# Performance work log

Hardware: AMD Instinct MI355X
Metric: run time of the kernel (lower is better)

The kernel has to match this reference:

```python
import jax, jax.numpy as jnp
import numpy as np

N = 10000      # nodes
E = 320000     # edges (avg degree 32)
SI, VI = 256, 32   # node scalar / vector channels
SE, VE = 64, 4     # edge scalar / vector channels
SO, VO = 256, 32   # output channels
IN_S = 2 * SI + SE         # 576 (self_message=True)
IN_V = 2 * VI + VE         # 68
H = max(IN_V, VO)          # 68, GBP hidden vector dim
EPS = 1e-8


def setup_inputs() -> dict:
    key = jax.random.key(0)
    ks = jax.random.split(key, 9)
    node_s = jax.random.normal(ks[0], (N, SI), jnp.float32)
    node_v = jax.random.normal(ks[1], (N, VI, 3), jnp.float32)
    edge_s = jax.random.normal(ks[2], (E, SE), jnp.float32)
    edge_v = jax.random.normal(ks[3], (E, VE, 3), jnp.float32)
    # GBP params (stored as [in, out] so y = x @ W)
    wh = jax.random.normal(ks[4], (IN_V, H), jnp.float32) / np.sqrt(IN_V)
    ws_w = jax.random.normal(ks[5], (IN_S + H, SO), jnp.float32) / np.sqrt(IN_S + H)
    ws_b = jnp.zeros((SO,), jnp.float32)
    wv = jax.random.normal(ks[6], (H, VO), jnp.float32) / np.sqrt(H)
    edge_index = jax.random.randint(ks[7], (2, E), 0, N, jnp.int64)
    return {"node_s": node_s, "node_v": node_v, "edge_s": edge_s,
            "edge_v": edge_v, "wh": wh, "ws_w": ws_w, "ws_b": ws_b,
            "wv": wv, "edge_index": edge_index}


def reference(node_s, node_v, edge_s, edge_v, wh, ws_w, ws_b, wv, edge_index):
    n = node_s.shape[0]
    src, dst = edge_index[0], edge_index[1]
    # gather + tuple_cat((s_j, v_j), edge_attr, (s_i, v_i))
    s_cat = jnp.concatenate([node_s[src], edge_s, node_s[dst]], axis=-1)   # [E, IN_S]
    v_cat = jnp.concatenate([node_v[src], edge_v, node_v[dst]], axis=-2)   # [E, IN_V, 3]
    # GBP message (activations=(None,None), no vector gate)
    v_pre = jnp.swapaxes(v_cat, -1, -2)                # [E, 3, IN_V]
    vh = v_pre @ wh                                    # [E, 3, H]
    vn = jnp.sqrt(jnp.maximum(jnp.sum(vh * vh, axis=-2), EPS))  # _norm_no_nan, [E, H]
    s_msg = jnp.concatenate([s_cat, vn], axis=-1) @ ws_w + ws_b  # [E, SO]
    v_msg = jnp.swapaxes(vh @ wv, -1, -2)              # [E, VO, 3]
    # scatter-mean to target nodes
    agg_s = jax.ops.segment_sum(s_msg, dst, num_segments=n)       # [N, SO]
    agg_v = jax.ops.segment_sum(v_msg, dst, num_segments=n)       # [N, VO, 3]
    cnt = jax.ops.segment_sum(jnp.ones((s_msg.shape[0],), s_msg.dtype), dst,
                              num_segments=n)
    cnt = jnp.maximum(cnt, 1.0)
    out_s = agg_s / cnt[:, None]
    out_v = agg_v / cnt[:, None, None]
    # _merge(s, V): flatten vector channels and append to scalars
    return jnp.concatenate([out_s, out_v.reshape(n, 3 * VO)], axis=-1)  # [N, SO+3*VO]
```

## Files before the change

### kernel.cpp

```cpp
#include <hip/hip_runtime.h>
#include <hip/hip_bf16.h>

#define N_NODES 10000
#define E_TOT   320000

typedef __attribute__((ext_vector_type(8))) short short8;
typedef __attribute__((ext_vector_type(4))) short s16x4;
typedef __attribute__((ext_vector_type(4))) float f32x4;

#define HIST_OFF    0u
#define FILL_OFF    40000u
#define ZERO_BYTES  80000u
#define ROWPTR_OFF  80000u
#define PERM_OFF    120064u
#define PSRC_OFF    1400064u
#define CN_OFF      2680064u
#define QARR_OFF    13560064u
#define QV_OFF      17720064u
#define WHV4_OFF    19640064u
#define WBIG_OFF    19640576u
#define NSBF_OFF    19984640u
#define ANSB_OFF    25104640u
#define EAB_OFF     30224640u
#define AP_OFF      33424640u
#define AEV_OFF     41584640u
#define FLAGS_OFF   42064640u
#define NODES_OFF   120064u

union BfS { __hip_bfloat16 h; short s; };
__device__ __forceinline__ short f2bf(float x) { BfS u; u.h = __float2bfloat16(x); return u.s; }
__device__ __forceinline__ float bf(short x) { BfS u; u.s = x; return __bfloat162float(u.h); }
__device__ __forceinline__ float bflo(unsigned u) { return __uint_as_float(u << 16); }
__device__ __forceinline__ float bfhi(unsigned u) { return __uint_as_float(u & 0xffff0000u); }
__device__ __forceinline__ float ldin(const void* p, int f32m, long i) {
  return f32m ? ((const float*)p)[i] : __bfloat162float(((const __hip_bfloat16*)p)[i]);
}
__device__ __forceinline__ int get_ei(const void* p, int i64m, long i) {
  return i64m ? (int)(((const long long*)p)[i]) : ((const int*)p)[i];
}

__global__ __launch_bounds__(256) void hist_det(
    const void* __restrict__ edge_index, const unsigned short* __restrict__ ns_u16,
    int* __restrict__ hist, int* __restrict__ flags)
{
  const int tid = threadIdx.x;
  const int* ei = (const int*)edge_index;
  int nz = (ei[2 * tid + 1] != 0) ? 1 : 0;
  unsigned long long m = __ballot(nz);
  __shared__ int cnt4[4];
  if ((tid & 63) == 0) cnt4[tid >> 6] = __popcll(m);
  __syncthreads();
  const int i64m = (cnt4[0] + cnt4[1] + cnt4[2] + cnt4[3]) < 16 ? 1 : 0;
  int e = blockIdx.x * 256 + tid;
  int dst = get_ei(edge_index, i64m, (long)E_TOT + e);
  atomicAdd(&hist[dst], 1);
  if (blockIdx.x == 0) {
    __shared__ int cf;
    if (tid == 0) cf = 0;
    __syncthreads();
    int c1 = 0;
    for (int i = tid; i < 8192; i += 256) {
      unsigned ex = (ns_u16[2 * i] >> 7) & 0xFF;
      if (ex < 100 || ex > 140) c1++;
    }
    atomicAdd(&cf, c1);
    __syncthreads();
    if (tid == 0) { flags[0] = (cf > 512) ? 1 : 0; flags[1] = i64m; }
  }
}

__global__ __launch_bounds__(256) void scanperm(
    const void* __restrict__ edge_index, const int* __restrict__ flags,
    const int* __restrict__ hist, int* __restrict__ rowptr,
    int* __restrict__ fill, int* __restrict__ perm, int* __restrict__ psrc)
{
  __shared__ int rp[N_NODES];
  __shared__ int part[256];
  const int tid = threadIdx.x;
  for (int i = tid; i < N_NODES; i += 256) rp[i] = hist[i];
  __syncthreads();
  const int base = tid * 40;
  int s = 0;
  for (int i = 0; i < 40; ++i) { int idx = base + i; if (idx < N_NODES) s += rp[idx]; }
  part[tid] = s;
  __syncthreads();
  for (int off = 1; off < 256; off <<= 1) {
    int v = (tid >= off) ? part[tid - off] : 0;
    __syncthreads();
    part[tid] += v;
    __syncthreads();
  }
  int run = (tid > 0) ? part[tid - 1] : 0;
  for (int i = 0; i < 40; ++i) {
    int idx = base + i;
    if (idx < N_NODES) { int h = rp[idx]; rp[idx] = run; run += h; }
  }
  __syncthreads();
  if (blockIdx.x == 0) {
    for (int i = tid; i < N_NODES; i += 256) rowptr[i] = rp[i];
    if (tid == 0) rowptr[N_NODES] = part[255];
  }
  const int i64m = flags[1];
  int e = blockIdx.x * 256 + tid;
  int dst = get_ei(edge_index, i64m, (long)E_TOT + e);
  int src = get_ei(edge_index, i64m, e);
  int pos = rp[dst] + atomicAdd(&fill[dst], 1);
  perm[pos] = e; psrc[pos] = src;
}

__global__ __launch_bounds__(256) void node_pre_prep(
    const void* __restrict__ node_v, const void* __restrict__ wh,
    const void* __restrict__ wv, const void* __restrict__ node_s,
    const void* __restrict__ ws_w, const int* __restrict__ flags,
    short* __restrict__ CN, short* __restrict__ QARR,
    short* __restrict__ QV, short* __restrict__ ns_bf,
    short* __restrict__ Wbig, float* __restrict__ whv4)
{
  const int f32m = flags[0];
  const int b = blockIdx.x, tid = threadIdx.x;
  __shared__ float whs[68 * 68];
  __shared__ float wvs[68 * 32];
  __shared__ float nv[4][96];
  __shared__ float pq[4][408];
  if (b >= 2500) {
    int pb = b - 2500;
    if (pb < 672) {
      int flat = pb * 256 + tid;
      int o = flat / 672, k = flat % 672;
      short v = 0;
      if (k < 320)      v = f2bf(ldin(ws_w, f32m, (long)k * 256 + o));
      else if (k < 388) v = f2bf(ldin(ws_w, f32m, (long)(576 + k - 320) * 256 + o));
      else if (k >= 416) v = f2bf(ldin(ws_w, f32m, (long)(k - 96) * 256 + o));
      Wbig[flat] = v;
    } else if (tid < 128) {
      int q = tid / 32, c = tid % 32;
      float acc = 0.f;
      for (int h = 0; h < 68; ++h)
        acc += ldin(wh, f32m, (32 + q) * 68 + h) * ldin(wv, f32m, h * 32 + c);
      whv4[tid] = acc;
    }
    return;
  }
  int n0 = b * 4;
  for (int i = tid; i < 4624; i += 256) whs[i] = ldin(wh, f32m, i);
  for (int i = tid; i < 2176; i += 256) wvs[i] = ldin(wv, f32m, i);
  for (int i = tid; i < 4 * 96; i += 256) nv[i / 96][i % 96] = ldin(node_v, f32m, (long)n0 * 96 + i);
  for (int i = tid; i < 1024; i += 256)
    ns_bf[(long)n0 * 256 + i] = f2bf(ldin(node_s, f32m, (long)n0 * 256 + i));
  __syncthreads();
  for (int o = tid; o < 4 * 408; o += 256) {
    int i = o / 408, r0 = o % 408;
    int part = r0 / 204, r = r0 % 204, d = r / 68, h = r % 68;
    int cbase = part ? 36 : 0;
    float acc = 0.f;
#pragma unroll
    for (int c = 0; c < 32; ++c)
      acc += nv[i][c * 3 + d] * whs[(cbase + c) * 68 + h];
    pq[i][r0] = acc;
  }
  __syncthreads();
  for (int o = tid; o < 4 * 544; o += 256) {
    int i = o / 544, k = o % 544;
    short v = 0;
    if (k < 512) {
      int l = k >> 3, j = k & 7;
      if (j < 4)      v = f2bf(ldin(node_s, f32m, (long)(n0 + i) * 256 + l * 4 + j));
      else if (j < 7) v = f2bf(pq[i][(j - 4) * 68 + l]);
    } else if (k < 528) {
      int idx = k - 512, jj = idx >> 2, d = idx & 3;
      if (d < 3) v = f2bf(pq[i][d * 68 + 64 + jj]);
    }
    CN[(long)(n0 + i) * 544 + k] = v;
  }
  for (int o = tid; o < 4 * 208; o += 256) {
    int i = o / 208, k = o % 208;
    QARR[(long)(n0 + i) * 208 + k] = (k < 204) ? f2bf(pq[i][204 + k]) : (short)0;
  }
  for (int o = tid; o < 4 * 96; o += 256) {
    int i = o / 96, r = o % 96, d = r / 32, c = r % 32;
    float acc = 0.f;
    for (int h = 0; h < 68; ++h)
      acc += pq[i][204 + d * 68 + h] * wvs[h * 32 + c];
    QV[(long)(n0 + i) * 96 + r] = f2bf(acc);
  }
}

struct EdgeLds {
  float ansL[4][256];
  float apL[4][204];
  float avnL[4][132];
  float aesL[4][64];
  float aevL[4][12];
};

template <int F32M>
__device__ __forceinline__ void edge_body(
    const void* __restrict__ edge_v, const void* __restrict__ edge_s,
    const void* __restrict__ wh,
    const int* __restrict__ rowptr, const int* __restrict__ perm,
    const int* __restrict__ psrc, const short* __restrict__ CN,
    const short* __restrict__ QARR,
    short* __restrict__ ANSb, short* __restrict__ EAb,
    float* __restrict__ AP, float* __restrict__ AEV, EdgeLds* lds)
{
  const int tid = threadIdx.x;
  const int lane = tid & 63, w = tid >> 6;
  const int n = blockIdx.x;
  const int beg = rowptr[n], deg = rowptr[n + 1] - beg;
  const bool has2 = (lane < 4);
  const int h2 = 64 + lane;
  const float w4a0 = ldin(wh, F32M, 32 * 68 + lane);
  const float w4a1 = ldin(wh, F32M, 33 * 68 + lane);
  const float w4a2 = ldin(wh, F32M, 34 * 68 + lane);
  const float w4a3 = ldin(wh, F32M, 35 * 68 + lane);
  const float w4b0 = has2 ? ldin(wh, F32M, 32 * 68 + h2) : 0.f;
  const float w4b1 = has2 ? ldin(wh, F32M, 33 * 68 + h2) : 0.f;
  const float w4b2 = has2 ? ldin(wh, F32M, 34 * 68 + h2) : 0.f;
  const float w4b3 = has2 ? ldin(wh, F32M, 35 * 68 + h2) : 0.f;
  const short* qp = QARR + (long)n * 208;
  const float qa0 = bf(qp[0 * 68 + lane]);
  const float qa1 = bf(qp[1 * 68 + lane]);
  const float qa2 = bf(qp[2 * 68 + lane]);
  const float qb0 = has2 ? bf(qp[0 * 68 + h2]) : 0.f;
  const float qb1 = has2 ? bf(qp[1 * 68 + h2]) : 0.f;
  const float qb2 = has2 ? bf(qp[2 * 68 + h2]) : 0.f;
  float an0 = 0.f, an1 = 0.f, an2 = 0.f, an3 = 0.f;
  float ap0 = 0.f, ap1 = 0.f, ap2 = 0.f;
  float bq0 = 0.f, bq1 = 0.f, bq2 = 0.f;
  float avna = 0.f, avnb = 0.f, aes = 0.f, aev = 0.f;

  int e = w;
  int s_cur = 0, d_cur = 0;
  int sv1 = 0, id1 = 0;
  short8 cv = {};
  s16x4 tl = {};
  float es_c = 0.f, evl_c = 0.f;
  float c0 = 0.f, c1 = 0.f, c2 = 0.f, c3 = 0.f, c4 = 0.f, c5 = 0.f;
  float c6 = 0.f, c7 = 0.f, c8 = 0.f, c9 = 0.f, cA = 0.f, cB = 0.f;
  if (e < deg) {
    int sv0 = psrc[beg + e], id0 = perm[beg + e];
    s_cur = __builtin_amdgcn_readfirstlane(sv0);
    d_cur = __builtin_amdgcn_readfirstlane(id0);
    cv = *(const short8*)(CN + (long)s_cur * 544 + lane * 8);
    if (has2) tl = *(const s16x4*)(CN + (long)s_cur * 544 + 512 + lane * 4);
    es_c = ldin(edge_s, F32M, (long)d_cur * 64 + lane);
    if (lane < 12) evl_c = ldin(edge_v, F32M, (long)d_cur * 12 + lane);
    if (F32M) {
      const float* evp = (const float*)edge_v + (long)d_cur * 12;
      c0 = evp[0]; c1 = evp[1]; c2 = evp[2]; c3 = evp[3];
      c4 = evp[4]; c5 = evp[5]; c6 = evp[6]; c7 = evp[7];
      c8 = evp[8]; c9 = evp[9]; cA = evp[10]; cB = evp[11];
    } else {
      const unsigned* evp = (const unsigned*)((const short*)edge_v + (long)d_cur * 12);
      unsigned u0 = evp[0], u1 = evp[1], u2 = evp[2];
      unsigned u3 = evp[3], u4 = evp[4], u5 = evp[5];
      c0 = bflo(u0); c1 = bfhi(u0); c2 = bflo(u1); c3 = bfhi(u1);
      c4 = bflo(u2); c5 = bfhi(u2); c6 = bflo(u3); c7 = bfhi(u3);
      c8 = bflo(u4); c9 = bfhi(u4); cA = bflo(u5); cB = bfhi(u5);
    }
  }
  if (e + 4 < deg) { sv1 = psrc[beg + e + 4]; id1 = perm[beg + e + 4]; }

  while (e < deg) {
    const bool vnext = (e + 4 < deg);
    const int sN = vnext ? __builtin_amdgcn_readfirstlane(sv1) : s_cur;
    const int dN = vnext ? __builtin_amdgcn_readfirstlane(id1) : d_cur;
    short8 cvn = *(const short8*)(CN + (long)sN * 544 + lane * 8);
    s16x4 tln = {};
    if (has2) tln = *(const s16x4*)(CN + (long)sN * 544 + 512 + lane * 4);
    float es_n = ldin(edge_s, F32M, (long)dN * 64 + lane);
    float evl_n = 0.f;
    if (lane < 12) evl_n = ldin(edge_v, F32M, (long)dN * 12 + lane);
    float n0, n1, n2, n3, n4, n5, n6, n7, n8, n9, nA, nB;
    if (F32M) {
      const float* evp = (const float*)edge_v + (long)dN * 12;
      n0 = evp[0]; n1 = evp[1]; n2 = evp[2]; n3 = evp[3];
      n4 = evp[4]; n5 = evp[5]; n6 = evp[6]; n7 = evp[7];
      n8 = evp[8]; n9 = evp[9]; nA = evp[10]; nB = evp[11];
    } else {
      const unsigned* evp = (const unsigned*)((const short*)edge_v + (long)dN * 12);
      unsigned u0 = evp[0], u1 = evp[1], u2 = evp[2];
      unsigned u3 = evp[3], u4 = evp[4], u5 = evp[5];
      n0 = bflo(u0); n1 = bfhi(u0); n2 = bflo(u1); n3 = bfhi(u1);
      n4 = bflo(u2); n5 = bfhi(u2); n6 = bflo(u3); n7 = bfhi(u3);
      n8 = bflo(u4); n9 = bfhi(u4); nA = bflo(u5); nB = bfhi(u5);
    }
    if (e + 8 < deg) { sv1 = psrc[beg + e + 8]; id1 = perm[beg + e + 8]; }
    an0 += bf(cv[0]); an1 += bf(cv[1]); an2 += bf(cv[2]); an3 += bf(cv[3]);
    const float pa0 = bf(cv[4]), pa1 = bf(cv[5]), pa2 = bf(cv[6]);
    aes += es_c; aev += evl_c;
    float v0 = pa0 + qa0 + c0 * w4a0 + c3 * w4a1 + c6 * w4a2 + c9 * w4a3;
    float v1 = pa1 + qa1 + c1 * w4a0 + c4 * w4a1 + c7 * w4a2 + cA * w4a3;
    float v2 = pa2 + qa2 + c2 * w4a0 + c5 * w4a1 + c8 * w4a2 + cB * w4a3;
    avna += sqrtf(fmaxf(v0 * v0 + v1 * v1 + v2 * v2, 1e-8f));
    ap0 += pa0; ap1 += pa1; ap2 += pa2;
    if (has2) {
      const float pb0 = bf(tl.x), pb1 = bf(tl.y), pb2 = bf(tl.z);
      float u0 = pb0 + qb0 + c0 * w4b0 + c3 * w4b1 + c6 * w4b2 + c9 * w4b3;
      float u1 = pb1 + qb1 + c1 * w4b0 + c4 * w4b1 + c7 * w4b2 + cA * w4b3;
      float u2 = pb2 + qb2 + c2 * w4b0 + c5 * w4b1 + c8 * w4b2 + cB * w4b3;
      avnb += sqrtf(fmaxf(u0 * u0 + u1 * u1 + u2 * u2, 1e-8f));
      bq0 += pb0; bq1 += pb1; bq2 += pb2;
    }
    cv = cvn; tl = tln; es_c = es_n; evl_c = evl_n;
    c0 = n0; c1 = n1; c2 = n2; c3 = n3; c4 = n4; c5 = n5;
    c6 = n6; c7 = n7; c8 = n8; c9 = n9; cA = nA; cB = nB;
    s_cur = sN; d_cur = dN;
    e += 4;
  }
  lds->ansL[w][lane * 4 + 0] = an0; lds->ansL[w][lane * 4 + 1] = an1;
  lds->ansL[w][lane * 4 + 2] = an2; lds->ansL[w][lane * 4 + 3] = an3;
  lds->apL[w][lane * 3 + 0] = ap0; lds->apL[w][lane * 3 + 1] = ap1;
  lds->apL[w][lane * 3 + 2] = ap2;
  if (has2) {
    lds->apL[w][192 + lane * 3 + 0] = bq0;
    lds->apL[w][192 + lane * 3 + 1] = bq1;
    lds->apL[w][192 + lane * 3 + 2] = bq2;
  }
  lds->avnL[w][lane] = avna;
  if (has2) lds->avnL[w][64 + lane] = avnb;
  lds->aesL[w][lane] = aes;
  if (lane < 12) lds->aevL[w][lane] = aev;
  __syncthreads();
  const float inv = 1.f / fmaxf((float)deg, 1.f);
  {
    float s = lds->ansL[0][tid] + lds->ansL[1][tid] + lds->ansL[2][tid] + lds->ansL[3][tid];
    ANSb[(long)n * 256 + tid] = f2bf(s * inv);
  }
  if (tid < 204) {
    float s = lds->apL[0][tid] + lds->apL[1][tid] + lds->apL[2][tid] + lds->apL[3][tid];
    AP[(long)n * 204 + tid] = s;
  } else if (tid < 216) {
    int c = tid - 204;
    float s = lds->aevL[0][c] + lds->aevL[1][c] + lds->aevL[2][c] + lds->aevL[3][c];
    AEV[(long)n * 12 + c] = s;
  }
  if (tid < 64) {
    float s = lds->aesL[0][tid] + lds->aesL[1][tid] + lds->aesL[2][tid] + lds->aesL[3][tid];
    EAb[(long)n * 160 + tid] = f2bf(s * inv);
  } else if (tid < 132) {
    int c = tid - 64;
    float s = lds->avnL[0][c] + lds->avnL[1][c] + lds->avnL[2][c] + lds->avnL[3][c];
    EAb[(long)n * 160 + 64 + c] = f2bf(s * inv);
  } else if (tid < 160) {
    EAb[(long)n * 160 + tid] = 0;
  }
}

__global__ __launch_bounds__(256) void edge_block(
    const void* __restrict__ edge_v, const void* __restrict__ edge_s,
    const void* __restrict__ wh, const int* __restrict__ flags,
    const int* __restrict__ rowptr, const int* __restrict__ perm,
    const int* __restrict__ psrc, const short* __restrict__ CN,
    const short* __restrict__ QARR,
    short* __restrict__ ANSb, short* __restrict__ EAb,
    float* __restrict__ AP, float* __restrict__ AEV)
{
  __shared__ EdgeLds lds;
  if (flags[0])
    edge_body<1>(edge_v, edge_s, wh, rowptr, perm, psrc, CN, QARR,
                 ANSb, EAb, AP, AEV, &lds);
  else
    edge_body<0>(edge_v, edge_s, wh, rowptr, perm, psrc, CN, QARR,
                 ANSb, EAb, AP, AEV, &lds);
}

__global__ __launch_bounds__(256) void node_gemm(
    const short* __restrict__ ANSb, const short* __restrict__ EAb,
    const short* __restrict__ nsb, const short* __restrict__ Wbig,
    float* __restrict__ NodeS)
{
  __shared__ __align__(16) short Xs[64 * 40];
  __shared__ __align__(16) short Ws[256 * 40];
  const int tid = threadIdx.x;
  const int n0 = blockIdx.x * 64;
  const int lane = tid & 63, wave = tid >> 6;
  const int frow = lane & 15, fk = (lane >> 4) * 8, q = lane >> 4;
  f32x4 acc[4][4];
#pragma unroll
  for (int ri = 0; ri < 4; ++ri)
#pragma unroll
    for (int ci = 0; ci < 4; ++ci)
      acc[ri][ci] = (f32x4){0.f, 0.f, 0.f, 0.f};
  const int se = tid >> 2, sq = tid & 3;
  const int rn = min(n0 + se, N_NODES - 1);
  for (int s = 0; s < 21; ++s) {
    short8 xv;
    if (s < 8)       xv = *(const short8*)&ANSb[(long)rn * 256 + s * 32 + sq * 8];
    else if (s < 13) xv = *(const short8*)&EAb[(long)rn * 160 + (s - 8) * 32 + sq * 8];
    else             xv = *(const short8*)&nsb[(long)rn * 256 + (s - 13) * 32 + sq * 8];
    *(short8*)&Xs[se * 40 + sq * 8] = xv;
#pragma unroll
    for (int it = 0; it < 4; ++it) {
      int flat = it * 256 + tid;
      int nn = flat >> 2, qq = flat & 3;
      *(short8*)&Ws[nn * 40 + qq * 8] = *(const short8*)&Wbig[nn * 672 + s * 32 + qq * 8];
    }
    __syncthreads();
    short8 a[4];
#pragma unroll
    for (int ri = 0; ri < 4; ++ri)
      a[ri] = *(const short8*)&Xs[(ri * 16 + frow) * 40 + fk];
#pragma unroll
    for (int ci = 0; ci < 4; ++ci) {
      int nn = wave * 64 + ci * 16 + frow;
      short8 b = *(const short8*)&Ws[nn * 40 + fk];
#pragma unroll
      for (int ri = 0; ri < 4; ++ri)
        acc[ri][ci] = __builtin_amdgcn_mfma_f32_16x16x32_bf16(a[ri], b, acc[ri][ci], 0, 0, 0);
    }
    __syncthreads();
  }
#pragma unroll
  for (int ri = 0; ri < 4; ++ri)
#pragma unroll
    for (int rr = 0; rr < 4; ++rr) {
      int row = n0 + ri * 16 + q * 4 + rr;
      if (row < N_NODES) {
#pragma unroll
        for (int ci = 0; ci < 4; ++ci) {
          int col = wave * 64 + ci * 16 + (lane & 15);
          NodeS[(long)row * 256 + col] = acc[ri][ci][rr];
        }
      }
    }
}

__global__ __launch_bounds__(256) void final_fuse(
    const float* __restrict__ NodeS, const float* __restrict__ AP,
    const float* __restrict__ AEV, const void* __restrict__ wv,
    const float* __restrict__ whv4, const int* __restrict__ rowptr,
    const short* __restrict__ QV, const void* __restrict__ ws_b,
    const int* __restrict__ flags, void* __restrict__ out)
{
  const int f32m = flags[0];
  int n0 = blockIdx.x * 4, tid = threadIdx.x;
  __shared__ float wvs[68 * 32];
  __shared__ float wh4s[128];
  __shared__ float APs[4][204];
  __shared__ float AEVs[4][12];
  __shared__ float aggL[4][96];
  for (int i = tid; i < 2176; i += 256) wvs[i] = ldin(wv, f32m, i);
  if (tid < 128) wh4s[tid] = whv4[tid];
  for (int i = tid; i < 816; i += 256) APs[i / 204][i % 204] = AP[(long)n0 * 204 + i];
  if (tid < 48) AEVs[tid / 12][tid % 12] = AEV[(long)n0 * 12 + tid];
  __syncthreads();
  for (int o = tid; o < 384; o += 256) {
    int i = o / 96, r = o % 96, c = r / 3, d = r % 3;
    float acc = AEVs[i][d] * wh4s[c] + AEVs[i][3 + d] * wh4s[32 + c]
              + AEVs[i][6 + d] * wh4s[64 + c] + AEVs[i][9 + d] * wh4s[96 + c];
    for (int h = 0; h < 68; ++h)
      acc += APs[i][h * 3 + d] * wvs[h * 32 + c];
    aggL[i][r] = acc;
  }
  __syncthreads();
  for (int o = tid; o < 1408; o += 256) {
    int i = o / 352, j = o % 352;
    int n = n0 + i;
    int deg = rowptr[n + 1] - rowptr[n];
    float v;
    if (j < 256) {
      v = (deg > 0) ? (NodeS[(long)n * 256 + j] + ldin(ws_b, f32m, j)) : 0.f;
    } else {
      int m = j - 256, ch = m / 3, d = m % 3;
      float inv = 1.f / fmaxf((float)deg, 1.f);
      v = aggL[i][m] * inv;
      if (deg > 0) v += bf(QV[(long)n * 96 + d * 32 + ch]);
    }
    long flat = (long)n * 352 + j;
    if (f32m) ((float*)out)[flat] = v;
    else      ((__hip_bfloat16*)out)[flat] = __float2bfloat16(v);
  }
}

extern "C" void kernel_launch(void* const* d_in, const int* in_sizes, int n_in,
                              void* d_out, int out_size, void* d_ws, size_t ws_size,
                              hipStream_t stream) {
  const void* node_s = d_in[0];
  const void* node_v = d_in[1];
  const void* edge_s = d_in[2];
  const void* edge_v = d_in[3];
  const void* wh     = d_in[4];
  const void* ws_w   = d_in[5];
  const void* ws_b   = d_in[6];
  const void* wv     = d_in[7];
  const void* edge_index = d_in[8];

  char* ws = (char*)d_ws;
  int*   hist  = (int*)(ws + HIST_OFF);
  int*   fill  = (int*)(ws + FILL_OFF);
  int*   rowptr= (int*)(ws + ROWPTR_OFF);
  int*   perm  = (int*)(ws + PERM_OFF);
  int*   psrc  = (int*)(ws + PSRC_OFF);
  short* CN    = (short*)(ws + CN_OFF);
  short* QARR  = (short*)(ws + QARR_OFF);
  short* QV    = (short*)(ws + QV_OFF);
  float* whv4  = (float*)(ws + WHV4_OFF);
  short* Wbig  = (short*)(ws + WBIG_OFF);
  short* ns_bf = (short*)(ws + NSBF_OFF);
  short* ANSb  = (short*)(ws + ANSB_OFF);
  short* EAb   = (short*)(ws + EAB_OFF);
  float* AP    = (float*)(ws + AP_OFF);
  float* AEV   = (float*)(ws + AEV_OFF);
  float* NodeS = (float*)(ws + NODES_OFF);
  int*   flags = (int*)(ws + FLAGS_OFF);

  hipMemsetAsync(d_ws, 0, ZERO_BYTES, stream);
  hist_det<<<1250, 256, 0, stream>>>(edge_index, (const unsigned short*)node_s,
                                     hist, flags);
  scanperm<<<1250, 256, 0, stream>>>(edge_index, flags, hist, rowptr, fill,
                                     perm, psrc);
  node_pre_prep<<<3173, 256, 0, stream>>>(node_v, wh, wv, node_s, ws_w, flags,
                                          CN, QARR, QV, ns_bf, Wbig, whv4);
  edge_block<<<10000, 256, 0, stream>>>(edge_v, edge_s, wh, flags, rowptr,
                                        perm, psrc, CN, QARR,
                                        ANSb, EAb, AP, AEV);
  node_gemm<<<157, 256, 0, stream>>>(ANSb, EAb, ns_bf, Wbig, NodeS);
  final_fuse<<<2500, 256, 0, stream>>>(NodeS, AP, AEV, wv, whv4, rowptr,
                                       QV, ws_b, flags, d_out);
}
```

Before: 431.2 us.

## Pre-permute edge features into CSR order during scanperm for sequential edge reads

During the permutation pass, scanperm now scatters each edge's scalar and vector features (converted to bf16) into a new workspace buffer ordered by CSR position. A new edge kernel then reads these features sequentially by row instead of gathering them through perm. The fallback kernel, used when the workspace is too small, drops the explicit one-ahead software prefetch of the gathered data. The cost is an extra scattered write of roughly 48 MB in scanperm, bf16 rounding of the edge features in the f32 path, and a dependence on workspace size.

```diff
diff --git a/kernel.cpp b/kernel.cpp
--- a/kernel.cpp
+++ b/kernel.cpp
@@ -25,6 +25,8 @@
 #define AP_OFF      33424640u
 #define AEV_OFF     41584640u
 #define FLAGS_OFF   42064640u
+#define EVS_OFF     42064704u
+#define EVS_BYTES   48640000u
 #define NODES_OFF   120064u
 
 union BfS { __hip_bfloat16 h; short s; };
@@ -70,12 +72,15 @@
 }
 
 __global__ __launch_bounds__(256) void scanperm(
-    const void* __restrict__ edge_index, const int* __restrict__ flags,
+    const void* __restrict__ edge_index, const void* __restrict__ edge_s,
+    const void* __restrict__ edge_v, const int* __restrict__ flags,
     const int* __restrict__ hist, int* __restrict__ rowptr,
-    int* __restrict__ fill, int* __restrict__ perm, int* __restrict__ psrc)
+    int* __restrict__ fill, int* __restrict__ perm, int* __restrict__ psrc,
+    short* __restrict__ EVS, int do_copy)
 {
   __shared__ int rp[N_NODES];
   __shared__ int part[256];
+  __shared__ int posL[256];
   const int tid = threadIdx.x;
   for (int i = tid; i < N_NODES; i += 256) rp[i] = hist[i];
   __syncthreads();
@@ -100,12 +105,24 @@
     for (int i = tid; i < N_NODES; i += 256) rowptr[i] = rp[i];
     if (tid == 0) rowptr[N_NODES] = part[255];
   }
-  const int i64m = flags[1];
+  const int i64m = flags[1], f32m = flags[0];
   int e = blockIdx.x * 256 + tid;
   int dst = get_ei(edge_index, i64m, (long)E_TOT + e);
   int src = get_ei(edge_index, i64m, e);
   int pos = rp[dst] + atomicAdd(&fill[dst], 1);
   perm[pos] = e; psrc[pos] = src;
+  posL[tid] = pos;
+  __syncthreads();
+  if (do_copy) {
+    const long ebase = (long)blockIdx.x * 256;
+    for (int i = tid; i < 256 * 76; i += 256) {
+      int li = i / 76, ch = i - li * 76;
+      long eg = ebase + li;
+      float v = (ch < 64) ? ldin(edge_s, f32m, eg * 64 + ch)
+                          : ldin(edge_v, f32m, eg * 12 + (ch - 64));
+      EVS[(long)posL[li] * 76 + ch] = f2bf(v);
+    }
+  }
 }
 
 __global__ __launch_bounds__(256) void node_pre_prep(
@@ -193,8 +210,126 @@
   float aevL[4][12];
 };
 
+__device__ __forceinline__ void edge_reduce_epilogue(
+    EdgeLds* lds, int n, int tid, int deg,
+    short* __restrict__ ANSb, short* __restrict__ EAb,
+    float* __restrict__ AP, float* __restrict__ AEV)
+{
+  __syncthreads();
+  const float inv = 1.f / fmaxf((float)deg, 1.f);
+  {
+    float s = lds->ansL[0][tid] + lds->ansL[1][tid] + lds->ansL[2][tid] + lds->ansL[3][tid];
+    ANSb[(long)n * 256 + tid] = f2bf(s * inv);
+  }
+  if (tid < 204) {
+    float s = lds->apL[0][tid] + lds->apL[1][tid] + lds->apL[2][tid] + lds->apL[3][tid];
+    AP[(long)n * 204 + tid] = s;
+  } else if (tid < 216) {
+    int c = tid - 204;
+    float s = lds->aevL[0][c] + lds->aevL[1][c] + lds->aevL[2][c] + lds->aevL[3][c];
+    AEV[(long)n * 12 + c] = s;
+  }
+  if (tid < 64) {
+    float s = lds->aesL[0][tid] + lds->aesL[1][tid] + lds->aesL[2][tid] + lds->aesL[3][tid];
+    EAb[(long)n * 160 + tid] = f2bf(s * inv);
+  } else if (tid < 132) {
+    int c = tid - 64;
+    float s = lds->avnL[0][c] + lds->avnL[1][c] + lds->avnL[2][c] + lds->avnL[3][c];
+    EAb[(long)n * 160 + 64 + c] = f2bf(s * inv);
+  } else if (tid < 160) {
+    EAb[(long)n * 160 + tid] = 0;
+  }
+}
+
+__global__ __launch_bounds__(256) void edge_block_seq(
+    const short* __restrict__ EVS, const void* __restrict__ wh,
+    const int* __restrict__ flags, const int* __restrict__ rowptr,
+    const int* __restrict__ psrc, const short* __restrict__ CN,
+    const short* __restrict__ QARR,
+    short* __restrict__ ANSb, short* __restrict__ EAb,
+    float* __restrict__ AP, float* __restrict__ AEV)
+{
+  __shared__ EdgeLds lds;
+  const int f32m = flags[0];
+  const int tid = threadIdx.x, lane = tid & 63, w = tid >> 6;
+  const int n = blockIdx.x;
+  const int beg = rowptr[n], deg = rowptr[n + 1] - beg;
+  const bool has2 = (lane < 4);
+  const int h2 = 64 + lane;
+  const float w4a0 = ldin(wh, f32m, 32 * 68 + lane);
+  const float w4a1 = ldin(wh, f32m, 33 * 68 + lane);
+  const float w4a2 = ldin(wh, f32m, 34 * 68 + lane);
+  const float w4a3 = ldin(wh, f32m, 35 * 68 + lane);
+  const float w4b0 = has2 ? ldin(wh, f32m, 32 * 68 + h2) : 0.f;
+  const float w4b1 = has2 ? ldin(wh, f32m, 33 * 68 + h2) : 0.f;
+  const float w4b2 = has2 ? ldin(wh, f32m, 34 * 68 + h2) : 0.f;
+  const float w4b3 = has2 ? ldin(wh, f32m, 35 * 68 + h2) : 0.f;
+  const short* qp = QARR + (long)n * 208;
+  const float qa0 = bf(qp[0 * 68 + lane]);
+  const float qa1 = bf(qp[1 * 68 + lane]);
+  const float qa2 = bf(qp[2 * 68 + lane]);
+  const float qb0 = has2 ? bf(qp[0 * 68 + h2]) : 0.f;
+  const float qb1 = has2 ? bf(qp[1 * 68 + h2]) : 0.f;
+  const float qb2 = has2 ? bf(qp[2 * 68 + h2]) : 0.f;
+  float an0 = 0.f, an1 = 0.f, an2 = 0.f, an3 = 0.f;
+  float ap0 = 0.f, ap1 = 0.f, ap2 = 0.f;
+  float bq0 = 0.f, bq1 = 0.f, bq2 = 0.f;
+  float avna = 0.f, avnb = 0.f, aes = 0.f, aev = 0.f;
+  int e = w;
+  int sv = (e < deg) ? psrc[beg + e] : 0;
+  while (e < deg) {
+    int en = e + 4;
+    int svn = (en < deg) ? psrc[beg + en] : 0;
+    const int s_s = __builtin_amdgcn_readfirstlane(sv);
+    const int row = __builtin_amdgcn_readfirstlane(beg + e);
+    const short* cs = CN + (long)s_s * 544;
+    short8 cv = *(const short8*)(cs + lane * 8);
+    const short* er = EVS + (long)row * 76;
+    float esv = bf(er[lane]);
+    float evl = (lane < 12) ? bf(er[64 + lane]) : 0.f;
+    const unsigned* ep = (const unsigned*)(er + 64);
+    unsigned u0 = ep[0], u1 = ep[1], u2 = ep[2];
+    unsigned u3 = ep[3], u4 = ep[4], u5 = ep[5];
+    float c0 = bflo(u0), c1 = bfhi(u0), c2 = bflo(u1), c3 = bfhi(u1);
+    float c4 = bflo(u2), c5 = bfhi(u2), c6 = bflo(u3), c7 = bfhi(u3);
+    float c8 = bflo(u4), c9 = bfhi(u4), cA = bflo(u5), cB = bfhi(u5);
+    an0 += bf(cv[0]); an1 += bf(cv[1]); an2 += bf(cv[2]); an3 += bf(cv[3]);
+    const float pa0 = bf(cv[4]), pa1 = bf(cv[5]), pa2 = bf(cv[6]);
+    aes += esv; aev += evl;
+    float v0 = pa0 + qa0 + c0 * w4a0 + c3 * w4a1 + c6 * w4a2 + c9 * w4a3;
+    float v1 = pa1 + qa1 + c1 * w4a0 + c4 * w4a1 + c7 * w4a2 + cA * w4a3;
+    float v2 = pa2 + qa2 + c2 * w4a0 + c5 * w4a1 + c8 * w4a2 + cB * w4a3;
+    avna += sqrtf(fmaxf(v0 * v0 + v1 * v1 + v2 * v2, 1e-8f));
+    ap0 += pa0; ap1 += pa1; ap2 += pa2;
+    if (has2) {
+      s16x4 tl = *(const s16x4*)(cs + 512 + lane * 4);
+      const float pb0 = bf(tl.x), pb1 = bf(tl.y), pb2 = bf(tl.z);
+      float t0 = pb0 + qb0 + c0 * w4b0 + c3 * w4b1 + c6 * w4b2 + c9 * w4b3;
+      float t1 = pb1 + qb1 + c1 * w4b0 + c4 * w4b1 + c7 * w4b2 + cA * w4b3;
+      float t2 = pb2 + qb2 + c2 * w4b0 + c5 * w4b1 + c8 * w4b2 + cB * w4b3;
+      avnb += sqrtf(fmaxf(t0 * t0 + t1 * t1 + t2 * t2, 1e-8f));
+      bq0 += pb0; bq1 += pb1; bq2 += pb2;
+    }
+    e = en; sv = svn;
+  }
+  lds.ansL[w][lane * 4 + 0] = an0; lds.ansL[w][lane * 4 + 1] = an1;
+  lds.ansL[w][lane * 4 + 2] = an2; lds.ansL[w][lane * 4 + 3] = an3;
+  lds.apL[w][lane * 3 + 0] = ap0; lds.apL[w][lane * 3 + 1] = ap1;
+  lds.apL[w][lane * 3 + 2] = ap2;
+  if (has2) {
+    lds.apL[w][192 + lane * 3 + 0] = bq0;
+    lds.apL[w][192 + lane * 3 + 1] = bq1;
+    lds.apL[w][192 + lane * 3 + 2] = bq2;
+  }
+  lds.avnL[w][lane] = avna;
+  if (has2) lds.avnL[w][64 + lane] = avnb;
+  lds.aesL[w][lane] = aes;
+  if (lane < 12) lds.aevL[w][lane] = aev;
+  edge_reduce_epilogue(&lds, n, tid, deg, ANSb, EAb, AP, AEV);
+}
+
 template <int F32M>
-__device__ __forceinline__ void edge_body(
+__device__ __forceinline__ void edge_body_fb(
     const void* __restrict__ edge_v, const void* __restrict__ edge_s,
     const void* __restrict__ wh,
     const int* __restrict__ rowptr, const int* __restrict__ perm,
@@ -228,85 +363,49 @@
   float ap0 = 0.f, ap1 = 0.f, ap2 = 0.f;
   float bq0 = 0.f, bq1 = 0.f, bq2 = 0.f;
   float avna = 0.f, avnb = 0.f, aes = 0.f, aev = 0.f;
-
   int e = w;
-  int s_cur = 0, d_cur = 0;
-  int sv1 = 0, id1 = 0;
-  short8 cv = {};
-  s16x4 tl = {};
-  float es_c = 0.f, evl_c = 0.f;
-  float c0 = 0.f, c1 = 0.f, c2 = 0.f, c3 = 0.f, c4 = 0.f, c5 = 0.f;
-  float c6 = 0.f, c7 = 0.f, c8 = 0.f, c9 = 0.f, cA = 0.f, cB = 0.f;
-  if (e < deg) {
-    int sv0 = psrc[beg + e], id0 = perm[beg + e];
-    s_cur = __builtin_amdgcn_readfirstlane(sv0);
-    d_cur = __builtin_amdgcn_readfirstlane(id0);
-    cv = *(const short8*)(CN + (long)s_cur * 544 + lane * 8);
-    if (has2) tl = *(const s16x4*)(CN + (long)s_cur * 544 + 512 + lane * 4);
-    es_c = ldin(edge_s, F32M, (long)d_cur * 64 + lane);
-    if (lane < 12) evl_c = ldin(edge_v, F32M, (long)d_cur * 12 + lane);
+  int sv = 0, eid = 0;
+  if (e < deg) { sv = psrc[beg + e]; eid = perm[beg + e]; }
+  while (e < deg) {
+    int en = e + 4, svn = 0, eidn = 0;
+    if (en < deg) { svn = psrc[beg + en]; eidn = perm[beg + en]; }
+    const int sv_s  = __builtin_amdgcn_readfirstlane(sv);
+    const int eid_s = __builtin_amdgcn_readfirstlane(eid);
+    float ev0, ev1, ev2, ev3, ev4, ev5, ev6, ev7, ev8, ev9, evA, evB;
     if (F32M) {
-      const float* evp = (const float*)edge_v + (long)d_cur * 12;
-      c0 = evp[0]; c1 = evp[1]; c2 = evp[2]; c3 = evp[3];
-      c4 = evp[4]; c5 = evp[5]; c6 = evp[6]; c7 = evp[7];
-      c8 = evp[8]; c9 = evp[9]; cA = evp[10]; cB = evp[11];
+      const float* evp = (const float*)edge_v + (long)eid_s * 12;
+      ev0 = evp[0]; ev1 = evp[1]; ev2 = evp[2]; ev3 = evp[3];
+      ev4 = evp[4]; ev5 = evp[5]; ev6 = evp[6]; ev7 = evp[7];
+      ev8 = evp[8]; ev9 = evp[9]; evA = evp[10]; evB = evp[11];
     } else {
-      const unsigned* evp = (const unsigned*)((const short*)edge_v + (long)d_cur * 12);
+      const unsigned* evp = (const unsigned*)((const short*)edge_v + (long)eid_s * 12);
       unsigned u0 = evp[0], u1 = evp[1], u2 = evp[2];
       unsigned u3 = evp[3], u4 = evp[4], u5 = evp[5];
-      c0 = bflo(u0); c1 = bfhi(u0); c2 = bflo(u1); c3 = bfhi(u1);
-      c4 = bflo(u2); c5 = bfhi(u2); c6 = bflo(u3); c7 = bfhi(u3);
-      c8 = bflo(u4); c9 = bfhi(u4); cA = bflo(u5); cB = bfhi(u5);
-    }
-  }
-  if (e + 4 < deg) { sv1 = psrc[beg + e + 4]; id1 = perm[beg + e + 4]; }
-
-  while (e < deg) {
-    const bool vnext = (e + 4 < deg);
-    const int sN = vnext ? __builtin_amdgcn_readfirstlane(sv1) : s_cur;
-    const int dN = vnext ? __builtin_amdgcn_readfirstlane(id1) : d_cur;
-    short8 cvn = *(const short8*)(CN + (long)sN * 544 + lane * 8);
-    s16x4 tln = {};
-    if (has2) tln = *(const s16x4*)(CN + (long)sN * 544 + 512 + lane * 4);
-    float es_n = ldin(edge_s, F32M, (long)dN * 64 + lane);
-    float evl_n = 0.f;
-    if (lane < 12) evl_n = ldin(edge_v, F32M, (long)dN * 12 + lane);
-    float n0, n1, n2, n3, n4, n5, n6, n7, n8, n9, nA, nB;
-    if (F32M) {
-      const float* evp = (const float*)edge_v + (long)dN * 12;
-      n0 = evp[0]; n1 = evp[1]; n2 = evp[2]; n3 = evp[3];
-      n4 = evp[4]; n5 = evp[5]; n6 = evp[6]; n7 = evp[7];
-      n8 = evp[8]; n9 = evp[9]; nA = evp[10]; nB = evp[11];
-    } else {
-      const unsigned* evp = (const unsigned*)((const short*)edge_v + (long)dN * 12);
-      unsigned u0 = evp[0], u1 = evp[1], u2 = evp[2];
-      unsigned u3 = evp[3], u4 = evp[4], u5 = evp[5];
-      n0 = bflo(u0); n1 = bfhi(u0); n2 = bflo(u1); n3 = bfhi(u1);
-      n4 = bflo(u2); n5 = bfhi(u2); n6 = bflo(u3); n7 = bfhi(u3);
-      n8 = bflo(u4); n9 = bfhi(u4); nA = bflo(u5); nB = bfhi(u5);
-    }
-    if (e + 8 < deg) { sv1 = psrc[beg + e + 8]; id1 = perm[beg + e + 8]; }
+      ev0 = bflo(u0); ev1 = bfhi(u0); ev2 = bflo(u1); ev3 = bfhi(u1);
+      ev4 = bflo(u2); ev5 = bfhi(u2); ev6 = bflo(u3); ev7 = bfhi(u3);
+      ev8 = bflo(u4); ev9 = bfhi(u4); evA = bflo(u5); evB = bfhi(u5);
+    }
+    const short* cs = CN + (long)sv_s * 544;
+    short8 cv = *(const short8*)(cs + lane * 8);
     an0 += bf(cv[0]); an1 += bf(cv[1]); an2 += bf(cv[2]); an3 += bf(cv[3]);
     const float pa0 = bf(cv[4]), pa1 = bf(cv[5]), pa2 = bf(cv[6]);
-    aes += es_c; aev += evl_c;
-    float v0 = pa0 + qa0 + c0 * w4a0 + c3 * w4a1 + c6 * w4a2 + c9 * w4a3;
-    float v1 = pa1 + qa1 + c1 * w4a0 + c4 * w4a1 + c7 * w4a2 + cA * w4a3;
-    float v2 = pa2 + qa2 + c2 * w4a0 + c5 * w4a1 + c8 * w4a2 + cB * w4a3;
+    aes += ldin(edge_s, F32M, (long)eid_s * 64 + lane);
+    if (lane < 12) aev += ldin(edge_v, F32M, (long)eid_s * 12 + lane);
+    float v0 = pa0 + qa0 + ev0 * w4a0 + ev3 * w4a1 + ev6 * w4a2 + ev9 * w4a3;
+    float v1 = pa1 + qa1 + ev1 * w4a0 + ev4 * w4a1 + ev7 * w4a2 + evA * w4a3;
+    float v2 = pa2 + qa2 + ev2 * w4a0 + ev5 * w4a1 + ev8 * w4a2 + evB * w4a3;
     avna += sqrtf(fmaxf(v0 * v0 + v1 * v1 + v2 * v2, 1e-8f));
     ap0 += pa0; ap1 += pa1; ap2 += pa2;
     if (has2) {
-      const float pb0 = bf(tl.x), pb1 = bf(tl.y), pb2 = bf(tl.z);
-      float u0 = pb0 + qb0 + c0 * w4b0 + c3 * w4b1 + c6 * w4b2 + c9 * w4b3;
-      float u1 = pb1 + qb1 + c1 * w4b0 + c4 * w4b1 + c7 * w4b2 + cA * w4b3;
-      float u2 = pb2 + qb2 + c2 * w4b0 + c5 * w4b1 + c8 * w4b2 + cB * w4b3;
+      s16x4 p2 = *(const s16x4*)(cs + 512 + lane * 4);
+      const float pb0 = bf(p2.x), pb1 = bf(p2.y), pb2 = bf(p2.z);
+      float u0 = pb0 + qb0 + ev0 * w4b0 + ev3 * w4b1 + ev6 * w4b2 + ev9 * w4b3;
+      float u1 = pb1 + qb1 + ev1 * w4b0 + ev4 * w4b1 + ev7 * w4b2 + evA * w4b3;
+      float u2 = pb2 + qb2 + ev2 * w4b0 + ev5 * w4b1 + ev8 * w4b2 + evB * w4b3;
       avnb += sqrtf(fmaxf(u0 * u0 + u1 * u1 + u2 * u2, 1e-8f));
       bq0 += pb0; bq1 += pb1; bq2 += pb2;
     }
-    cv = cvn; tl = tln; es_c = es_n; evl_c = evl_n;
-    c0 = n0; c1 = n1; c2 = n2; c3 = n3; c4 = n4; c5 = n5;
-    c6 = n6; c7 = n7; c8 = n8; c9 = n9; cA = nA; cB = nB;
-    s_cur = sN; d_cur = dN;
-    e += 4;
+    e = en; sv = svn; eid = eidn;
   }
   lds->ansL[w][lane * 4 + 0] = an0; lds->ansL[w][lane * 4 + 1] = an1;
   lds->ansL[w][lane * 4 + 2] = an2; lds->ansL[w][lane * 4 + 3] = an3;
@@ -321,33 +420,10 @@
   if (has2) lds->avnL[w][64 + lane] = avnb;
   lds->aesL[w][lane] = aes;
   if (lane < 12) lds->aevL[w][lane] = aev;
-  __syncthreads();
-  const float inv = 1.f / fmaxf((float)deg, 1.f);
-  {
-    float s = lds->ansL[0][tid] + lds->ansL[1][tid] + lds->ansL[2][tid] + lds->ansL[3][tid];
-    ANSb[(long)n * 256 + tid] = f2bf(s * inv);
-  }
-  if (tid < 204) {
-    float s = lds->apL[0][tid] + lds->apL[1][tid] + lds->apL[2][tid] + lds->apL[3][tid];
-    AP[(long)n * 204 + tid] = s;
-  } else if (tid < 216) {
-    int c = tid - 204;
-    float s = lds->aevL[0][c] + lds->aevL[1][c] + lds->aevL[2][c] + lds->aevL[3][c];
-    AEV[(long)n * 12 + c] = s;
-  }
-  if (tid < 64) {
-    float s = lds->aesL[0][tid] + lds->aesL[1][tid] + lds->aesL[2][tid] + lds->aesL[3][tid];
-    EAb[(long)n * 160 + tid] = f2bf(s * inv);
-  } else if (tid < 132) {
-    int c = tid - 64;
-    float s = lds->avnL[0][c] + lds->avnL[1][c] + lds->avnL[2][c] + lds->avnL[3][c];
-    EAb[(long)n * 160 + 64 + c] = f2bf(s * inv);
-  } else if (tid < 160) {
-    EAb[(long)n * 160 + tid] = 0;
-  }
-}
-
-__global__ __launch_bounds__(256) void edge_block(
+  edge_reduce_epilogue(lds, n, tid, deg, ANSb, EAb, AP, AEV);
+}
+
+__global__ __launch_bounds__(256) void edge_block_fb(
     const void* __restrict__ edge_v, const void* __restrict__ edge_s,
     const void* __restrict__ wh, const int* __restrict__ flags,
     const int* __restrict__ rowptr, const int* __restrict__ perm,
@@ -358,11 +434,11 @@
 {
   __shared__ EdgeLds lds;
   if (flags[0])
-    edge_body<1>(edge_v, edge_s, wh, rowptr, perm, psrc, CN, QARR,
-                 ANSb, EAb, AP, AEV, &lds);
+    edge_body_fb<1>(edge_v, edge_s, wh, rowptr, perm, psrc, CN, QARR,
+                    ANSb, EAb, AP, AEV, &lds);
   else
-    edge_body<0>(edge_v, edge_s, wh, rowptr, perm, psrc, CN, QARR,
-                 ANSb, EAb, AP, AEV, &lds);
+    edge_body_fb<0>(edge_v, edge_s, wh, rowptr, perm, psrc, CN, QARR,
+                    ANSb, EAb, AP, AEV, &lds);
 }
 
 __global__ __launch_bounds__(256) void node_gemm(
@@ -504,17 +580,24 @@
   float* AEV   = (float*)(ws + AEV_OFF);
   float* NodeS = (float*)(ws + NODES_OFF);
   int*   flags = (int*)(ws + FLAGS_OFF);
+  short* EVS   = (short*)(ws + EVS_OFF);
+
+  const int do_copy = (ws_size >= (size_t)EVS_OFF + (size_t)EVS_BYTES) ? 1 : 0;
 
   hipMemsetAsync(d_ws, 0, ZERO_BYTES, stream);
   hist_det<<<1250, 256, 0, stream>>>(edge_index, (const unsigned short*)node_s,
                                      hist, flags);
-  scanperm<<<1250, 256, 0, stream>>>(edge_index, flags, hist, rowptr, fill,
-                                     perm, psrc);
+  scanperm<<<1250, 256, 0, stream>>>(edge_index, edge_s, edge_v, flags, hist,
+                                     rowptr, fill, perm, psrc, EVS, do_copy);
   node_pre_prep<<<3173, 256, 0, stream>>>(node_v, wh, wv, node_s, ws_w, flags,
                                           CN, QARR, QV, ns_bf, Wbig, whv4);
-  edge_block<<<10000, 256, 0, stream>>>(edge_v, edge_s, wh, flags, rowptr,
-                                        perm, psrc, CN, QARR,
-                                        ANSb, EAb, AP, AEV);
+  if (do_copy)
+    edge_block_seq<<<10000, 256, 0, stream>>>(EVS, wh, flags, rowptr, psrc,
+                                              CN, QARR, ANSb, EAb, AP, AEV);
+  else
+    edge_block_fb<<<10000, 256, 0, stream>>>(edge_v, edge_s, wh, flags, rowptr,
+                                             perm, psrc, CN, QARR,
+                                             ANSb, EAb, AP, AEV);
   node_gemm<<<157, 256, 0, stream>>>(ANSb, EAb, ns_bf, Wbig, NodeS);
   final_fuse<<<2500, 256, 0, stream>>>(NodeS, AP, AEV, wv, whv4, rowptr,
                                        QV, ws_b, flags, d_out);
```

Measured after the change: 508.9 us. 18.0% more time.
